# Performance work log

Measured on AMD Instinct MI355X. Metric: run time of the kernel, lower is better.

## Reference

```python
import jax, jax.numpy as jnp
import numpy as np

B, S, D, DFF = 4, 2048, 1024, 4096


def setup_inputs() -> dict:
    key = jax.random.key(0)
    ks = jax.random.split(key, 7)
    scale = 1.0 / np.sqrt(D)
    return {
        "x": jax.random.normal(ks[0], (B, S, D), dtype=jnp.float32),
        "wq": jax.random.normal(ks[1], (D, D), dtype=jnp.float32) * scale,
        "wk": jax.random.normal(ks[2], (D, D), dtype=jnp.float32) * scale,
        "wv": jax.random.normal(ks[3], (D, D), dtype=jnp.float32) * scale,
        "wo": jax.random.normal(ks[4], (D, D), dtype=jnp.float32) * scale,
        "w1": jax.random.normal(ks[5], (D, DFF), dtype=jnp.float32) * scale,
        "w2": jax.random.normal(ks[6], (DFF, D), dtype=jnp.float32) * (1.0 / np.sqrt(DFF)),
    }


def reference(x, wq, wk, wv, wo, w1, w2):
    # Single-head attention, NO 1/sqrt(d) scaling (faithful to source).
    q = x @ wq  # [B,S,D]
    k = x @ wk
    v = x @ wv
    scores = jnp.einsum("bsd,btd->bst", q, k)  # [B,S,S]
    weights = jax.nn.softmax(scores, axis=-1)
    attn = jnp.einsum("bst,btd->bsd", weights, v)
    proj = attn @ wo
    hidden = jax.nn.relu(proj @ w1)  # [B,S,DFF]
    out = hidden @ w2
    return out + x
```

## Files before the change

### kernel.cpp

```cpp
#include <hip/hip_runtime.h>
#include <hip/hip_bf16.h>
#include <hip/hip_fp16.h>


typedef _Float16 f16;
typedef __attribute__((ext_vector_type(8))) _Float16 f16x8;
typedef __attribute__((ext_vector_type(4))) _Float16 f16x4;
typedef __attribute__((ext_vector_type(4))) float f32x4;

#define BM 128
#define BN 128
#define BK 64

__device__ inline void gload16(const void* g, void* l) {
    __builtin_amdgcn_global_load_lds(
        (const __attribute__((address_space(1))) void*)g,
        (__attribute__((address_space(3))) void*)l, 16, 0, 0);
}

template<int EPI>
__global__ __launch_bounds__(256, 1)
void gemm_big(const f16* __restrict__ A, const f16* __restrict__ Bt,
              void* __restrict__ Cv,
              int K, int lda, int ldb, int ldc,
              long long sA, long long sB, long long sC)
{
    __shared__ f16 Ash[256 * BK];
    __shared__ f16 Bsh[256 * BK];

    const int t = threadIdx.x;
    const int z = blockIdx.z;
    A  += (size_t)z * sA;
    Bt += (size_t)z * sB;

    const int bm0 = blockIdx.x * 256;
    const int bn0 = blockIdx.y * 256;

    const int lane = t & 63;
    const int wid  = t >> 6;
    const int quad = lane >> 4;
    const int m16  = lane & 15;
    const int wm   = (wid & 1) * 128;
    const int wnn  = (wid >> 1) * 128;

    const int r0 = t >> 3;
    const int kc = ((t & 7) ^ (r0 & 7)) * 8;
    const char* gA0 = (const char*)(A  + (size_t)(bm0 + r0) * lda + kc);
    const char* gB0 = (const char*)(Bt + (size_t)(bn0 + r0) * ldb + kc);
    const long long aStep = 64LL * lda;
    const long long bStep = 64LL * ldb;
    char* lA = (char*)Ash + (wid << 10);
    char* lB = (char*)Bsh + (wid << 10);

    f32x4 acc[8][8] = {};

    const int nk = K / BK;
    #define ISSUE(kt) do { const long long ko = (long long)(kt) * 128;  \
        _Pragma("unroll")                                               \
        for (int ii = 0; ii < 8; ++ii) {                                \
            gload16(gA0 + ii * aStep + ko, lA + ii * 4096);             \
            gload16(gB0 + ii * bStep + ko, lB + ii * 4096);             \
        } } while (0)

    const int swz = m16 & 7;

    ISSUE(0);
    for (int kt = 0; kt < nk; ++kt) {
        __syncthreads();
        f16x8 af[2][8], bf[2][8];
        #pragma unroll
        for (int s = 0; s < 2; ++s) {
            const int ha = (((s << 2) | quad) ^ swz) * 8;
            #pragma unroll
            for (int i = 0; i < 8; ++i) {
                af[s][i] = *(const f16x8*)&Ash[(wm + i * 16 + m16) * BK + ha];
                bf[s][i] = *(const f16x8*)&Bsh[(wnn + i * 16 + m16) * BK + ha];
            }
        }
        __syncthreads();
        if (kt + 1 < nk) ISSUE(kt + 1);
        #pragma unroll
        for (int s = 0; s < 2; ++s)
            #pragma unroll
            for (int i = 0; i < 8; ++i)
                #pragma unroll
                for (int j = 0; j < 8; ++j)
                    acc[i][j] = __builtin_amdgcn_mfma_f32_16x16x32_f16(
                                    af[s][i], bf[s][j], acc[i][j], 0, 0, 0);
    }
    #undef ISSUE

    if (EPI <= 1) {
        f16* C = (f16*)Cv + (size_t)z * sC;
        #pragma unroll
        for (int i = 0; i < 8; ++i)
            #pragma unroll
            for (int ri = 0; ri < 4; ++ri) {
                const size_t row = (size_t)(bm0 + wm + i * 16 + quad * 4 + ri);
                f16* cp = C + row * ldc + (bn0 + wnn + m16);
                #pragma unroll
                for (int j = 0; j < 8; ++j) {
                    float v = acc[i][j][ri];
                    if (EPI == 1) v = fmaxf(v, 0.0f);
                    cp[j * 16] = (f16)v;
                }
            }
    } else {
        float* C = (float*)Cv + (size_t)z * sC;
        #pragma unroll
        for (int i = 0; i < 8; ++i)
            #pragma unroll
            for (int ri = 0; ri < 4; ++ri) {
                const size_t row = (size_t)(bm0 + wm + i * 16 + quad * 4 + ri);
                float* cp = C + row * ldc + (bn0 + wnn + m16);
                #pragma unroll
                for (int j = 0; j < 8; ++j)
                    cp[j * 16] = acc[i][j][ri];
            }
    }
}

template<int EPI>
__global__ __launch_bounds__(256, 2)
void gemm_f16(const f16* __restrict__ A, const f16* __restrict__ Bt,
              const float* __restrict__ Res, void* __restrict__ Cv,
              int K, int lda, int ldb, int ldc,
              long long sA, long long sB, long long sC)
{
    __shared__ char smem[32 * 1024];
    f16* Ash = (f16*)smem;
    f16* Bsh = (f16*)(smem + 16384);
    float* xbuf = (float*)smem;

    const int t = threadIdx.x;
    const int z = blockIdx.z;
    A  += (size_t)z * sA;
    Bt += (size_t)z * sB;

    const int bm0 = blockIdx.x * BM;
    const int bn0 = blockIdx.y * BN;

    const int lane = t & 63;
    const int wid  = t >> 6;
    const int quad = lane >> 4;
    const int m16  = lane & 15;
    const int ks   = wid & 1;
    const int wn64 = (wid >> 1) * 64;

    const int r0 = t >> 3;
    const int kc = ((t & 7) ^ (r0 & 7)) * 8;
    const char* gA[4]; const char* gB[4];
    #pragma unroll
    for (int i = 0; i < 4; ++i) {
        gA[i] = (const char*)(A  + (size_t)(bm0 + i * 32 + r0) * lda + kc);
        gB[i] = (const char*)(Bt + (size_t)(bn0 + i * 32 + r0) * ldb + kc);
    }
    char* lA = (char*)Ash + (wid << 10);
    char* lB = (char*)Bsh + (wid << 10);

    f32x4 acc[8][4] = {};

    const int nk = K / BK;
    #define ISSUE(kt) do { const int ko = (kt) * 128;   \
        gload16(gA[0] + ko, lA);                        \
        gload16(gA[1] + ko, lA + 4096);                 \
        gload16(gA[2] + ko, lA + 8192);                 \
        gload16(gA[3] + ko, lA + 12288);                \
        gload16(gB[0] + ko, lB);                        \
        gload16(gB[1] + ko, lB + 4096);                 \
        gload16(gB[2] + ko, lB + 8192);                 \
        gload16(gB[3] + ko, lB + 12288); } while (0)

    const int swz = m16 & 7;
    const int ha  = ((ks * 4 + quad) ^ swz) * 8;

    ISSUE(0);
    for (int kt = 0; kt < nk; ++kt) {
        __syncthreads();
        f16x8 af[8], bf[4];
        #pragma unroll
        for (int i = 0; i < 8; ++i)
            af[i] = *(const f16x8*)&Ash[(i * 16 + m16) * BK + ha];
        #pragma unroll
        for (int j = 0; j < 4; ++j)
            bf[j] = *(const f16x8*)&Bsh[(wn64 + j * 16 + m16) * BK + ha];
        __syncthreads();
        if (kt + 1 < nk) ISSUE(kt + 1);
        #pragma unroll
        for (int i = 0; i < 8; ++i)
            #pragma unroll
            for (int j = 0; j < 4; ++j)
                acc[i][j] = __builtin_amdgcn_mfma_f32_16x16x32_f16(
                                af[i], bf[j], acc[i][j], 0, 0, 0);
    }
    #undef ISSUE

    float* xb = xbuf + (wid >> 1) * 4096;
    #define XIDX(row, col) ((row) * 64 + ((col) ^ (((row) & 4) << 2)))
    if (ks == 1) {
        #pragma unroll
        for (int i = 0; i < 4; ++i)
            #pragma unroll
            for (int j = 0; j < 4; ++j)
                #pragma unroll
                for (int ri = 0; ri < 4; ++ri)
                    xb[XIDX(i * 16 + quad * 4 + ri, j * 16 + m16)] = acc[i][j][ri];
    }
    __syncthreads();
    if (ks == 0) {
        #pragma unroll
        for (int i = 0; i < 4; ++i)
            #pragma unroll
            for (int j = 0; j < 4; ++j)
                #pragma unroll
                for (int ri = 0; ri < 4; ++ri)
                    acc[i][j][ri] += xb[XIDX(i * 16 + quad * 4 + ri, j * 16 + m16)];
    }
    __syncthreads();
    if (ks == 0) {
        #pragma unroll
        for (int i = 0; i < 4; ++i)
            #pragma unroll
            for (int j = 0; j < 4; ++j)
                #pragma unroll
                for (int ri = 0; ri < 4; ++ri)
                    xb[XIDX(i * 16 + quad * 4 + ri, j * 16 + m16)] = acc[i + 4][j][ri];
    }
    __syncthreads();
    if (ks == 1) {
        #pragma unroll
        for (int i = 0; i < 4; ++i)
            #pragma unroll
            for (int j = 0; j < 4; ++j)
                #pragma unroll
                for (int ri = 0; ri < 4; ++ri)
                    acc[i + 4][j][ri] += xb[XIDX(i * 16 + quad * 4 + ri, j * 16 + m16)];
    }
    #undef XIDX

    #define STORE_TILE(IB, RB)                                                  \
        do {                                                                    \
            if (EPI <= 1) {                                                     \
                f16* C = (f16*)Cv + (size_t)z * sC;                             \
                _Pragma("unroll")                                               \
                for (int i = 0; i < 4; ++i)                                     \
                    _Pragma("unroll")                                           \
                    for (int ri = 0; ri < 4; ++ri) {                            \
                        const size_t row = (size_t)(bm0 + (RB) + i * 16 + quad * 4 + ri); \
                        f16* cp = C + row * ldc + (bn0 + wn64 + m16);           \
                        _Pragma("unroll")                                       \
                        for (int j = 0; j < 4; ++j) {                           \
                            float v = acc[(IB) + i][j][ri];                     \
                            if (EPI == 1) v = fmaxf(v, 0.0f);                   \
                            cp[j * 16] = (f16)v;                                \
                        }                                                       \
                    }                                                           \
            } else {                                                            \
                float* C = (float*)Cv + (size_t)z * sC;                         \
                _Pragma("unroll")                                               \
                for (int i = 0; i < 4; ++i)                                     \
                    _Pragma("unroll")                                           \
                    for (int ri = 0; ri < 4; ++ri) {                            \
                        const size_t row = (size_t)(bm0 + (RB) + i * 16 + quad * 4 + ri); \
                        float* cp = C + row * ldc + (bn0 + wn64 + m16);         \
                        const float* rp = (EPI == 3)                            \
                            ? Res + row * ldc + (bn0 + wn64 + m16) : nullptr;   \
                        _Pragma("unroll")                                       \
                        for (int j = 0; j < 4; ++j) {                           \
                            float v = acc[(IB) + i][j][ri];                     \
                            if (EPI == 3) v += rp[j * 16];                      \
                            cp[j * 16] = v;                                     \
                        }                                                       \
                    }                                                           \
            }                                                                   \
        } while (0)

    if (ks == 0) STORE_TILE(0, 0);
    else         STORE_TILE(4, 64);
    #undef STORE_TILE
}

__global__ __launch_bounds__(256)
void transpose_cast4(const float* __restrict__ s0, const float* __restrict__ s1,
                     const float* __restrict__ s2, const float* __restrict__ s3,
                     f16* __restrict__ d0, f16* __restrict__ d1,
                     f16* __restrict__ d2, f16* __restrict__ d3)
{
    const int R = 1024, C = 1024;
    const int z = blockIdx.z;
    const float* in = (z == 0) ? s0 : (z == 1) ? s1 : (z == 2) ? s2 : s3;
    f16* out = (z == 0) ? d0 : (z == 1) ? d1 : (z == 2) ? d2 : d3;
    __shared__ float tile[64][65];
    const int c0 = blockIdx.x * 64, r0 = blockIdx.y * 64;
    const int tc = threadIdx.x & 63, tr = threadIdx.x >> 6;
    #pragma unroll
    for (int i = 0; i < 16; ++i)
        tile[tr + i * 4][tc] = in[(size_t)(r0 + tr + i * 4) * C + c0 + tc];
    __syncthreads();
    #pragma unroll
    for (int i = 0; i < 16; ++i)
        out[(size_t)(c0 + tr + i * 4) * R + r0 + tc] = (f16)tile[tc][tr + i * 4];
}

__global__ __launch_bounds__(256)
void transpose_cast(const float* __restrict__ in, f16* __restrict__ out,
                    int R, int C)
{
    __shared__ float tile[64][65];
    const int c0 = blockIdx.x * 64, r0 = blockIdx.y * 64;
    const int tc = threadIdx.x & 63, tr = threadIdx.x >> 6;
    #pragma unroll
    for (int i = 0; i < 16; ++i)
        tile[tr + i * 4][tc] = in[(size_t)(r0 + tr + i * 4) * C + c0 + tc];
    __syncthreads();
    #pragma unroll
    for (int i = 0; i < 16; ++i)
        out[(size_t)(c0 + tr + i * 4) * R + r0 + tc] = (f16)tile[tc][tr + i * 4];
}

__global__ __launch_bounds__(256)
void cast_f16(const float* __restrict__ in, f16* __restrict__ out)
{
    const size_t i = ((size_t)blockIdx.x * 256 + threadIdx.x) * 4;
    float4 v = *(const float4*)(in + i);
    f16x4 o; o.x = (f16)v.x; o.y = (f16)v.y; o.z = (f16)v.z; o.w = (f16)v.w;
    *(f16x4*)(out + i) = o;
}

__global__ __launch_bounds__(256)
void softmax_f16(const float* __restrict__ S, f16* __restrict__ P)
{
    __shared__ float red[256];
    const float* p = S + (size_t)blockIdx.x * 2048;
    f16* q = P + (size_t)blockIdx.x * 2048;
    const int t = threadIdx.x;

    float4 u0 = *(const float4*)(p + t * 4);
    float4 u1 = *(const float4*)(p + 1024 + t * 4);

    float m = fmaxf(fmaxf(fmaxf(u0.x, u0.y), fmaxf(u0.z, u0.w)),
                    fmaxf(fmaxf(u1.x, u1.y), fmaxf(u1.z, u1.w)));
    red[t] = m;
    __syncthreads();
    #pragma unroll
    for (int s = 128; s > 0; s >>= 1) {
        if (t < s) red[t] = fmaxf(red[t], red[t + s]);
        __syncthreads();
    }
    const float rowmax = red[0];
    __syncthreads();

    u0.x = __expf(u0.x - rowmax); u0.y = __expf(u0.y - rowmax);
    u0.z = __expf(u0.z - rowmax); u0.w = __expf(u0.w - rowmax);
    u1.x = __expf(u1.x - rowmax); u1.y = __expf(u1.y - rowmax);
    u1.z = __expf(u1.z - rowmax); u1.w = __expf(u1.w - rowmax);

    red[t] = (u0.x + u0.y + u0.z + u0.w) + (u1.x + u1.y + u1.z + u1.w);
    __syncthreads();
    #pragma unroll
    for (int s = 128; s > 0; s >>= 1) {
        if (t < s) red[t] += red[t + s];
        __syncthreads();
    }
    const float inv = 1.0f / red[0];

    f16x4 o0, o1;
    o0.x = (f16)(u0.x * inv); o0.y = (f16)(u0.y * inv);
    o0.z = (f16)(u0.z * inv); o0.w = (f16)(u0.w * inv);
    o1.x = (f16)(u1.x * inv); o1.y = (f16)(u1.y * inv);
    o1.z = (f16)(u1.z * inv); o1.w = (f16)(u1.w * inv);
    *(f16x4*)(q + t * 4)        = o0;
    *(f16x4*)(q + 1024 + t * 4) = o1;
}

extern "C" void kernel_launch(void* const* d_in, const int* in_sizes, int n_in,
                              void* d_out, int out_size, void* d_ws, size_t ws_size,
                              hipStream_t stream)
{
    const float* x  = (const float*)d_in[0];
    const float* wq = (const float*)d_in[1];
    const float* wk = (const float*)d_in[2];
    const float* wv = (const float*)d_in[3];
    const float* wo = (const float*)d_in[4];
    const float* w1 = (const float*)d_in[5];
    const float* w2 = (const float*)d_in[6];
    float* out = (float*)d_out;

    const int S = 2048, D = 1024, DFF = 4096, Bb = 4;
    const int NTOK = Bb * S;

    f16* W    = (f16*)d_ws;
    f16* xh   = W;
    f16* wqkT = xh   + (size_t)NTOK * D;
    f16* wvT  = wqkT + (size_t)2 * D * D;
    f16* woT  = wvT  + (size_t)D * D;
    f16* w1T  = woT  + (size_t)D * D;
    f16* w2T  = w1T  + (size_t)D * DFF;
    f16* qk   = w2T  + (size_t)DFF * D;
    f16* vT   = qk   + (size_t)NTOK * 2 * D;
    float* sb = (float*)(vT + (size_t)D * NTOK);
    f16* ph   = qk;
    f16* at   = xh;
    f16* pj   = vT;
    f16* hd   = (f16*)sb;

    dim3 blk(256);

    cast_f16<<<dim3(NTOK * D / 1024), blk, 0, stream>>>(x, xh);
    transpose_cast4<<<dim3(D / 64, D / 64, 4), blk, 0, stream>>>(
        wq, wk, wv, wo, wqkT, wqkT + (size_t)D * D, wvT, woT);
    transpose_cast<<<dim3(DFF / 64, D / 64), blk, 0, stream>>>(w1, w1T, D, DFF);
    transpose_cast<<<dim3(D / 64, DFF / 64), blk, 0, stream>>>(w2, w2T, DFF, D);

    gemm_big<0><<<dim3(NTOK / 256, 2 * D / 256, 1), blk, 0, stream>>>(
        xh, wqkT, qk, D, D, D, 2 * D, 0, 0, 0);
    gemm_f16<0><<<dim3(D / BM, NTOK / BN, 1), blk, 0, stream>>>(
        wvT, xh, nullptr, vT, D, D, D, NTOK, 0, 0, 0);

    gemm_big<2><<<dim3(S / 256, S / 256, Bb), blk, 0, stream>>>(
        qk, qk + D, sb, D, 2 * D, 2 * D, S,
        (long long)S * 2 * D, (long long)S * 2 * D, (long long)S * S);

    softmax_f16<<<dim3(NTOK), blk, 0, stream>>>(sb, ph);

    gemm_f16<0><<<dim3(S / BM, D / BN, Bb), blk, 0, stream>>>(
        ph, vT, nullptr, at, S, S, NTOK, D,
        (long long)S * S, (long long)S, (long long)S * D);

    gemm_f16<0><<<dim3(NTOK / BM, D / BN, 1), blk, 0, stream>>>(
        at, woT, nullptr, pj, D, D, D, D, 0, 0, 0);

    gemm_big<1><<<dim3(NTOK / 256, DFF / 256, 1), blk, 0, stream>>>(
        pj, w1T, hd, D, D, D, DFF, 0, 0, 0);

    gemm_f16<3><<<dim3(NTOK / BM, D / BN, 1), blk, 0, stream>>>(
        hd, w2T, x, out, DFF, DFF, DFF, D, 0, 0, 0);
}
```

Measured before the change: 450.9 us.

## Fold Wq·Wkᵀ and Wv·Wo into precomputed weight products, drop separate K and projection GEMMs

Uses associativity to precompute Wq·Wkᵀ and Wv·Wo with a new split-K weight GEMM kernel. Scores then become (x·WqWkᵀ)·xᵀ, and the value path directly yields the output-projected values, which removes the K GEMM and the attention-output projection GEMM. Softmax now writes f16 in place over the float score buffer, and the large 256x256 GEMM kernel is replaced with 128x128 variants. The reassociated products are rounded to f16, which may change numerical error, and the in-place softmax needs the extra barrier that was added.

Result: faster. 427.6 us (-5.2%).

```diff
diff --git a/kernel.cpp b/kernel.cpp
--- a/kernel.cpp
+++ b/kernel.cpp
@@ -16,108 +16,6 @@
     __builtin_amdgcn_global_load_lds(
         (const __attribute__((address_space(1))) void*)g,
         (__attribute__((address_space(3))) void*)l, 16, 0, 0);
-}
-
-template<int EPI>
-__global__ __launch_bounds__(256, 1)
-void gemm_big(const f16* __restrict__ A, const f16* __restrict__ Bt,
-              void* __restrict__ Cv,
-              int K, int lda, int ldb, int ldc,
-              long long sA, long long sB, long long sC)
-{
-    __shared__ f16 Ash[256 * BK];
-    __shared__ f16 Bsh[256 * BK];
-
-    const int t = threadIdx.x;
-    const int z = blockIdx.z;
-    A  += (size_t)z * sA;
-    Bt += (size_t)z * sB;
-
-    const int bm0 = blockIdx.x * 256;
-    const int bn0 = blockIdx.y * 256;
-
-    const int lane = t & 63;
-    const int wid  = t >> 6;
-    const int quad = lane >> 4;
-    const int m16  = lane & 15;
-    const int wm   = (wid & 1) * 128;
-    const int wnn  = (wid >> 1) * 128;
-
-    const int r0 = t >> 3;
-    const int kc = ((t & 7) ^ (r0 & 7)) * 8;
-    const char* gA0 = (const char*)(A  + (size_t)(bm0 + r0) * lda + kc);
-    const char* gB0 = (const char*)(Bt + (size_t)(bn0 + r0) * ldb + kc);
-    const long long aStep = 64LL * lda;
-    const long long bStep = 64LL * ldb;
-    char* lA = (char*)Ash + (wid << 10);
-    char* lB = (char*)Bsh + (wid << 10);
-
-    f32x4 acc[8][8] = {};
-
-    const int nk = K / BK;
-    #define ISSUE(kt) do { const long long ko = (long long)(kt) * 128;  \
-        _Pragma("unroll")                                               \
-        for (int ii = 0; ii < 8; ++ii) {                                \
-            gload16(gA0 + ii * aStep + ko, lA + ii * 4096);             \
-            gload16(gB0 + ii * bStep + ko, lB + ii * 4096);             \
-        } } while (0)
-
-    const int swz = m16 & 7;
-
-    ISSUE(0);
-    for (int kt = 0; kt < nk; ++kt) {
-        __syncthreads();
-        f16x8 af[2][8], bf[2][8];
-        #pragma unroll
-        for (int s = 0; s < 2; ++s) {
-            const int ha = (((s << 2) | quad) ^ swz) * 8;
-            #pragma unroll
-            for (int i = 0; i < 8; ++i) {
-                af[s][i] = *(const f16x8*)&Ash[(wm + i * 16 + m16) * BK + ha];
-                bf[s][i] = *(const f16x8*)&Bsh[(wnn + i * 16 + m16) * BK + ha];
-            }
-        }
-        __syncthreads();
-        if (kt + 1 < nk) ISSUE(kt + 1);
-        #pragma unroll
-        for (int s = 0; s < 2; ++s)
-            #pragma unroll
-            for (int i = 0; i < 8; ++i)
-                #pragma unroll
-                for (int j = 0; j < 8; ++j)
-                    acc[i][j] = __builtin_amdgcn_mfma_f32_16x16x32_f16(
-                                    af[s][i], bf[s][j], acc[i][j], 0, 0, 0);
-    }
-    #undef ISSUE
-
-    if (EPI <= 1) {
-        f16* C = (f16*)Cv + (size_t)z * sC;
-        #pragma unroll
-        for (int i = 0; i < 8; ++i)
-            #pragma unroll
-            for (int ri = 0; ri < 4; ++ri) {
-                const size_t row = (size_t)(bm0 + wm + i * 16 + quad * 4 + ri);
-                f16* cp = C + row * ldc + (bn0 + wnn + m16);
-                #pragma unroll
-                for (int j = 0; j < 8; ++j) {
-                    float v = acc[i][j][ri];
-                    if (EPI == 1) v = fmaxf(v, 0.0f);
-                    cp[j * 16] = (f16)v;
-                }
-            }
-    } else {
-        float* C = (float*)Cv + (size_t)z * sC;
-        #pragma unroll
-        for (int i = 0; i < 8; ++i)
-            #pragma unroll
-            for (int ri = 0; ri < 4; ++ri) {
-                const size_t row = (size_t)(bm0 + wm + i * 16 + quad * 4 + ri);
-                float* cp = C + row * ldc + (bn0 + wnn + m16);
-                #pragma unroll
-                for (int j = 0; j < 8; ++j)
-                    cp[j * 16] = acc[i][j][ri];
-            }
-    }
 }
 
 template<int EPI>
@@ -280,26 +178,208 @@
     #undef STORE_TILE
 }
 
-__global__ __launch_bounds__(256)
-void transpose_cast4(const float* __restrict__ s0, const float* __restrict__ s1,
-                     const float* __restrict__ s2, const float* __restrict__ s3,
-                     f16* __restrict__ d0, f16* __restrict__ d1,
-                     f16* __restrict__ d2, f16* __restrict__ d3)
-{
-    const int R = 1024, C = 1024;
+template<int EPI>
+__global__ __launch_bounds__(256, 2)
+void gemm_ns(const f16* __restrict__ A, const f16* __restrict__ Bt,
+             void* __restrict__ Cv,
+             int K, int lda, int ldb, int ldc)
+{
+    __shared__ f16 Ash[BM * BK];
+    __shared__ f16 Bsh[BN * BK];
+
+    const int t = threadIdx.x;
+    const int bm0 = blockIdx.x * BM;
+    const int bn0 = blockIdx.y * BN;
+
+    const int lane = t & 63;
+    const int wid  = t >> 6;
+    const int quad = lane >> 4;
+    const int m16  = lane & 15;
+    const int wm = (wid & 1) * 64;
+    const int wn = (wid >> 1) * 64;
+
+    const int r0 = t >> 3;
+    const int kc = ((t & 7) ^ (r0 & 7)) * 8;
+    const char* gA[4]; const char* gB[4];
+    #pragma unroll
+    for (int i = 0; i < 4; ++i) {
+        gA[i] = (const char*)(A  + (size_t)(bm0 + i * 32 + r0) * lda + kc);
+        gB[i] = (const char*)(Bt + (size_t)(bn0 + i * 32 + r0) * ldb + kc);
+    }
+    char* lA = (char*)Ash + (wid << 10);
+    char* lB = (char*)Bsh + (wid << 10);
+
+    f32x4 acc[4][4] = {};
+
+    const int nk = K / BK;
+    #define ISSUE(kt) do { const int ko = (kt) * 128;   \
+        gload16(gA[0] + ko, lA);                        \
+        gload16(gA[1] + ko, lA + 4096);                 \
+        gload16(gA[2] + ko, lA + 8192);                 \
+        gload16(gA[3] + ko, lA + 12288);                \
+        gload16(gB[0] + ko, lB);                        \
+        gload16(gB[1] + ko, lB + 4096);                 \
+        gload16(gB[2] + ko, lB + 8192);                 \
+        gload16(gB[3] + ko, lB + 12288); } while (0)
+
+    const int swz = m16 & 7;
+
+    ISSUE(0);
+    for (int kt = 0; kt < nk; ++kt) {
+        __syncthreads();
+        f16x8 af[2][4], bf[2][4];
+        #pragma unroll
+        for (int s = 0; s < 2; ++s) {
+            const int ha = (((s << 2) | quad) ^ swz) * 8;
+            #pragma unroll
+            for (int i = 0; i < 4; ++i) {
+                af[s][i] = *(const f16x8*)&Ash[(wm + i * 16 + m16) * BK + ha];
+                bf[s][i] = *(const f16x8*)&Bsh[(wn + i * 16 + m16) * BK + ha];
+            }
+        }
+        __syncthreads();
+        if (kt + 1 < nk) ISSUE(kt + 1);
+        #pragma unroll
+        for (int s = 0; s < 2; ++s)
+            #pragma unroll
+            for (int i = 0; i < 4; ++i)
+                #pragma unroll
+                for (int j = 0; j < 4; ++j)
+                    acc[i][j] = __builtin_amdgcn_mfma_f32_16x16x32_f16(
+                                    af[s][i], bf[s][j], acc[i][j], 0, 0, 0);
+    }
+    #undef ISSUE
+
+    f16* C = (f16*)Cv;
+    #pragma unroll
+    for (int i = 0; i < 4; ++i)
+        #pragma unroll
+        for (int ri = 0; ri < 4; ++ri) {
+            const size_t row = (size_t)(bm0 + wm + i * 16 + quad * 4 + ri);
+            f16* cp = C + row * ldc + (bn0 + wn + m16);
+            #pragma unroll
+            for (int j = 0; j < 4; ++j) {
+                float v = acc[i][j][ri];
+                if (EPI == 1) v = fmaxf(v, 0.0f);
+                cp[j * 16] = (f16)v;
+            }
+        }
+}
+
+__global__ __launch_bounds__(256, 2)
+void gemm_dd(const f16* __restrict__ A0, const f16* __restrict__ B0, f16* __restrict__ C0,
+             const f16* __restrict__ A1, const f16* __restrict__ B1, f16* __restrict__ C1)
+{
+    const int LD = 1024;
+    __shared__ char smem[32 * 1024];
+    f16* Ash = (f16*)smem;
+    f16* Bsh = (f16*)(smem + 16384);
+    float* xred = (float*)smem;
+
+    const int t = threadIdx.x;
     const int z = blockIdx.z;
-    const float* in = (z == 0) ? s0 : (z == 1) ? s1 : (z == 2) ? s2 : s3;
-    f16* out = (z == 0) ? d0 : (z == 1) ? d1 : (z == 2) ? d2 : d3;
-    __shared__ float tile[64][65];
-    const int c0 = blockIdx.x * 64, r0 = blockIdx.y * 64;
-    const int tc = threadIdx.x & 63, tr = threadIdx.x >> 6;
-    #pragma unroll
-    for (int i = 0; i < 16; ++i)
-        tile[tr + i * 4][tc] = in[(size_t)(r0 + tr + i * 4) * C + c0 + tc];
-    __syncthreads();
-    #pragma unroll
-    for (int i = 0; i < 16; ++i)
-        out[(size_t)(c0 + tr + i * 4) * R + r0 + tc] = (f16)tile[tc][tr + i * 4];
+    const f16* A = z ? A1 : A0;
+    const f16* B = z ? B1 : B0;
+    f16* C = z ? C1 : C0;
+
+    const int bm0 = blockIdx.x * 64;
+    const int bn0 = blockIdx.y * 64;
+
+    const int lane = t & 63;
+    const int wid  = t >> 6;
+    const int quad = lane >> 4;
+    const int m16  = lane & 15;
+
+    const int rr = t >> 4;
+    const int kc = ((t & 15) ^ (rr & 15)) * 8;
+    const char* gA[4]; const char* gB[4];
+    #pragma unroll
+    for (int i = 0; i < 4; ++i) {
+        gA[i] = (const char*)(A + (size_t)(bm0 + i * 16 + rr) * LD + kc);
+        gB[i] = (const char*)(B + (size_t)(bn0 + i * 16 + rr) * LD + kc);
+    }
+    char* lA = (char*)Ash + (wid << 10);
+    char* lB = (char*)Bsh + (wid << 10);
+
+    f32x4 acc[4][4] = {};
+
+    #define ISSUE(kt) do { const int ko = (kt) * 256;   \
+        gload16(gA[0] + ko, lA);                        \
+        gload16(gA[1] + ko, lA + 4096);                 \
+        gload16(gA[2] + ko, lA + 8192);                 \
+        gload16(gA[3] + ko, lA + 12288);                \
+        gload16(gB[0] + ko, lB);                        \
+        gload16(gB[1] + ko, lB + 4096);                 \
+        gload16(gB[2] + ko, lB + 8192);                 \
+        gload16(gB[3] + ko, lB + 12288); } while (0)
+
+    const int sl = ((wid * 4 + quad) ^ m16) * 8;
+
+    ISSUE(0);
+    for (int kt = 0; kt < 8; ++kt) {
+        __syncthreads();
+        f16x8 af[4], bf[4];
+        #pragma unroll
+        for (int i = 0; i < 4; ++i) {
+            af[i] = *(const f16x8*)&Ash[(i * 16 + m16) * 128 + sl];
+            bf[i] = *(const f16x8*)&Bsh[(i * 16 + m16) * 128 + sl];
+        }
+        __syncthreads();
+        if (kt + 1 < 8) ISSUE(kt + 1);
+        #pragma unroll
+        for (int i = 0; i < 4; ++i)
+            #pragma unroll
+            for (int j = 0; j < 4; ++j)
+                acc[i][j] = __builtin_amdgcn_mfma_f32_16x16x32_f16(
+                                af[i], bf[j], acc[i][j], 0, 0, 0);
+    }
+    #undef ISSUE
+
+    #define XIDX(row, col) ((row) * 64 + ((col) ^ (((row) & 4) << 2)))
+    #define WR(base) do {                                                       \
+        _Pragma("unroll")                                                       \
+        for (int i = 0; i < 4; ++i)                                             \
+            _Pragma("unroll")                                                   \
+            for (int j = 0; j < 4; ++j)                                         \
+                _Pragma("unroll")                                               \
+                for (int ri = 0; ri < 4; ++ri)                                  \
+                    (base)[XIDX(i * 16 + quad * 4 + ri, j * 16 + m16)] = acc[i][j][ri]; \
+        } while (0)
+    #define RD(base) do {                                                       \
+        _Pragma("unroll")                                                       \
+        for (int i = 0; i < 4; ++i)                                             \
+            _Pragma("unroll")                                                   \
+            for (int j = 0; j < 4; ++j)                                         \
+                _Pragma("unroll")                                               \
+                for (int ri = 0; ri < 4; ++ri)                                  \
+                    acc[i][j][ri] += (base)[XIDX(i * 16 + quad * 4 + ri, j * 16 + m16)]; \
+        } while (0)
+
+    __syncthreads();
+    if (wid == 2) WR(xred);
+    if (wid == 3) WR(xred + 4096);
+    __syncthreads();
+    if (wid == 0) RD(xred);
+    if (wid == 1) RD(xred + 4096);
+    __syncthreads();
+    if (wid == 1) WR(xred);
+    __syncthreads();
+    if (wid == 0) {
+        RD(xred);
+        #pragma unroll
+        for (int i = 0; i < 4; ++i)
+            #pragma unroll
+            for (int ri = 0; ri < 4; ++ri) {
+                const size_t row = (size_t)(bm0 + i * 16 + quad * 4 + ri);
+                f16* cp = C + row * LD + (bn0 + m16);
+                #pragma unroll
+                for (int j = 0; j < 4; ++j)
+                    cp[j * 16] = (f16)acc[i][j][ri];
+            }
+    }
+    #undef WR
+    #undef RD
+    #undef XIDX
 }
 
 __global__ __launch_bounds__(256)
@@ -328,11 +408,25 @@
 }
 
 __global__ __launch_bounds__(256)
-void softmax_f16(const float* __restrict__ S, f16* __restrict__ P)
+void cast3_f16(const float* __restrict__ s0, const float* __restrict__ s1,
+               const float* __restrict__ s2,
+               f16* __restrict__ d0, f16* __restrict__ d1, f16* __restrict__ d2)
+{
+    const int z = blockIdx.z;
+    const float* in = (z == 0) ? s0 : (z == 1) ? s1 : s2;
+    f16* out = (z == 0) ? d0 : (z == 1) ? d1 : d2;
+    const size_t i = ((size_t)blockIdx.x * 256 + threadIdx.x) * 4;
+    float4 v = *(const float4*)(in + i);
+    f16x4 o; o.x = (f16)v.x; o.y = (f16)v.y; o.z = (f16)v.z; o.w = (f16)v.w;
+    *(f16x4*)(out + i) = o;
+}
+
+__global__ __launch_bounds__(256)
+void softmax_f16(float* __restrict__ S)
 {
     __shared__ float red[256];
-    const float* p = S + (size_t)blockIdx.x * 2048;
-    f16* q = P + (size_t)blockIdx.x * 2048;
+    float* p = S + (size_t)blockIdx.x * 2048;
+    f16* q = (f16*)p;
     const int t = threadIdx.x;
 
     float4 u0 = *(const float4*)(p + t * 4);
@@ -363,6 +457,7 @@
         __syncthreads();
     }
     const float inv = 1.0f / red[0];
+    __syncthreads();
 
     f16x4 o0, o1;
     o0.x = (f16)(u0.x * inv); o0.y = (f16)(u0.y * inv);
@@ -388,50 +483,53 @@
 
     const int S = 2048, D = 1024, DFF = 4096, Bb = 4;
     const int NTOK = Bb * S;
+    const size_t M1 = 1024 * 1024;
 
     f16* W    = (f16*)d_ws;
     f16* xh   = W;
-    f16* wqkT = xh   + (size_t)NTOK * D;
-    f16* wvT  = wqkT + (size_t)2 * D * D;
-    f16* woT  = wvT  + (size_t)D * D;
-    f16* w1T  = woT  + (size_t)D * D;
-    f16* w2T  = w1T  + (size_t)D * DFF;
-    f16* qk   = w2T  + (size_t)DFF * D;
-    f16* vT   = qk   + (size_t)NTOK * 2 * D;
-    float* sb = (float*)(vT + (size_t)D * NTOK);
-    f16* ph   = qk;
-    f16* at   = xh;
-    f16* pj   = vT;
-    f16* hd   = (f16*)sb;
+    f16* wqh  = W + 8 * M1;
+    f16* wkh  = W + 9 * M1;
+    f16* wvh  = W + 10 * M1;
+    f16* woT  = W + 11 * M1;
+    f16* w1T  = W + 12 * M1;
+    f16* w2T  = W + 16 * M1;
+    f16* wqkT = W + 20 * M1;
+    f16* wvoT = W + 21 * M1;
+    f16* qp   = W + 22 * M1;
+    f16* vwT  = W + 30 * M1;
+    float* sb = (float*)(W + 38 * M1);
+    f16* ph   = (f16*)sb;
+    f16* pj   = xh;
+    f16* hd   = qp;
 
     dim3 blk(256);
 
     cast_f16<<<dim3(NTOK * D / 1024), blk, 0, stream>>>(x, xh);
-    transpose_cast4<<<dim3(D / 64, D / 64, 4), blk, 0, stream>>>(
-        wq, wk, wv, wo, wqkT, wqkT + (size_t)D * D, wvT, woT);
+    cast3_f16<<<dim3(D * D / 1024, 1, 3), blk, 0, stream>>>(
+        wq, wk, wv, wqh, wkh, wvh);
+    transpose_cast<<<dim3(D / 64, D / 64), blk, 0, stream>>>(wo, woT, D, D);
     transpose_cast<<<dim3(DFF / 64, D / 64), blk, 0, stream>>>(w1, w1T, D, DFF);
     transpose_cast<<<dim3(D / 64, DFF / 64), blk, 0, stream>>>(w2, w2T, DFF, D);
-
-    gemm_big<0><<<dim3(NTOK / 256, 2 * D / 256, 1), blk, 0, stream>>>(
-        xh, wqkT, qk, D, D, D, 2 * D, 0, 0, 0);
+    gemm_dd<<<dim3(16, 16, 2), blk, 0, stream>>>(
+        wkh, wqh, wqkT, woT, wvh, wvoT);
+
+    gemm_f16<0><<<dim3(NTOK / BM, D / BN, 1), blk, 0, stream>>>(
+        xh, wqkT, nullptr, qp, D, D, D, D, 0, 0, 0);
     gemm_f16<0><<<dim3(D / BM, NTOK / BN, 1), blk, 0, stream>>>(
-        wvT, xh, nullptr, vT, D, D, D, NTOK, 0, 0, 0);
-
-    gemm_big<2><<<dim3(S / 256, S / 256, Bb), blk, 0, stream>>>(
-        qk, qk + D, sb, D, 2 * D, 2 * D, S,
-        (long long)S * 2 * D, (long long)S * 2 * D, (long long)S * S);
-
-    softmax_f16<<<dim3(NTOK), blk, 0, stream>>>(sb, ph);
+        wvoT, xh, nullptr, vwT, D, D, D, NTOK, 0, 0, 0);
+
+    gemm_f16<2><<<dim3(S / BM, S / BN, Bb), blk, 0, stream>>>(
+        qp, xh, nullptr, sb, D, D, D, S,
+        (long long)S * D, (long long)S * D, (long long)S * S);
+
+    softmax_f16<<<dim3(NTOK), blk, 0, stream>>>(sb);
 
     gemm_f16<0><<<dim3(S / BM, D / BN, Bb), blk, 0, stream>>>(
-        ph, vT, nullptr, at, S, S, NTOK, D,
-        (long long)S * S, (long long)S, (long long)S * D);
-
-    gemm_f16<0><<<dim3(NTOK / BM, D / BN, 1), blk, 0, stream>>>(
-        at, woT, nullptr, pj, D, D, D, D, 0, 0, 0);
-
-    gemm_big<1><<<dim3(NTOK / 256, DFF / 256, 1), blk, 0, stream>>>(
-        pj, w1T, hd, D, D, D, DFF, 0, 0, 0);
+        ph, vwT, nullptr, pj, S, 4096, NTOK, D,
+        (long long)S * 4096, (long long)S, (long long)S * D);
+
+    gemm_ns<1><<<dim3(NTOK / BM, DFF / BN, 1), blk, 0, stream>>>(
+        pj, w1T, hd, D, D, D, DFF);
 
     gemm_f16<3><<<dim3(NTOK / BM, D / BN, 1), blk, 0, stream>>>(
         hd, w2T, x, out, DFF, DFF, DFF, D, 0, 0, 0);
```
